# Kernel optimization log

Measured on AMD Instinct MI355X. Metric: run time of the kernel, lower is better.

The kernel has to match this reference:

```python
import jax, jax.numpy as jnp
import numpy as np

N = 500000   # query points
C = 10       # candidate faces per query (cand_num)
V = 100000   # mesh vertices
F = 200000   # mesh faces
EPS = 1e-9

def _dot(a, b):
    return jnp.sum(a * b, axis=-1)

def _proj_edge(v, e, p):
    # torch project_edge: dot(p - v, e) / clamp_min(dot(e, e), 1e-9)
    return _dot(p - v, e) / jnp.maximum(_dot(e, e), EPS)

def _is_not_above(v, e, n, p):
    # torch is_not_above: dot(cross(n, e), p - v) <= 0
    return _dot(jnp.cross(n, e), p - v) <= 0.0


def setup_inputs() -> dict:
    key = jax.random.key(0)
    k1, k2, k3, k4 = jax.random.split(key, 4)
    return {
        "query_xyz": jax.random.normal(k1, (N, 3), jnp.float32),
        "temp_verts": jax.random.normal(k2, (V, 3), jnp.float32),
        "faces": jax.random.randint(k3, (F, 3), 0, V),
        "cand_ids": jax.random.randint(k4, (N, C), 0, F),
    }


def _merged_distance(query_xyz, temp_verts, faces, cand_ids):
    # gather candidate face vertices: [N, C, 3(verts), 3(xyz)]
    fv = temp_verts[faces[cand_ids]]
    q = query_xyz[:, None, :]                       # [N, 1, 3]
    v0, v1, v2 = fv[:, :, 0, :], fv[:, :, 1, :], fv[:, :, 2, :]
    e10 = v1 - v0
    e21 = v2 - v1
    e02 = v0 - v2
    fN = -jnp.cross(e10, e02)                       # face normal (unnormalized)

    uab = _proj_edge(v0, e10, q)                    # [N, C]
    ubc = _proj_edge(v1, e21, q)
    uca = _proj_edge(v2, e02, q)

    t1 = (uca > 1.0) & (uab < 0.0)
    t2 = (uab > 1.0) & (ubc < 0.0)
    t3 = (ubc > 1.0) & (uca < 0.0)
    t4 = (uab >= 0.0) & (uab <= 1.0) & _is_not_above(v0, e10, fN, q)
    t5 = (ubc >= 0.0) & (ubc <= 1.0) & _is_not_above(v1, e21, fN, q) & ~t4
    t6 = (uca >= 0.0) & (uca <= 1.0) & _is_not_above(v2, e02, fN, q) & ~t4 & ~t5
    t0 = ~(t1 | t2 | t3 | t4 | t5 | t6)

    # type 0: signed distance to face plane (project_plane directed_dist)
    unit_n = fN / jnp.maximum(jnp.linalg.norm(fN, axis=-1, keepdims=True), EPS)
    d0 = _dot(q - v0, unit_n)

    # types 1-3: distance to vertices
    d1 = jnp.sqrt(jnp.sum((q - v0) ** 2, -1))
    d2 = jnp.sqrt(jnp.sum((q - v1) ** 2, -1))
    d3 = jnp.sqrt(jnp.sum((q - v2) ** 2, -1))

    # types 4-6: distance to edge projection points
    p4 = v0 + e10 * uab[..., None]
    p5 = v1 + e21 * ubc[..., None]
    p6 = v2 + e02 * uca[..., None]
    d4 = jnp.sqrt(jnp.sum((q - p4) ** 2, -1))
    d5 = jnp.sqrt(jnp.sum((q - p5) ** 2, -1))
    d6 = jnp.sqrt(jnp.sum((q - p6) ** 2, -1))

    f32 = lambda m: m.astype(d0.dtype)
    merged = (d0 * f32(t0) + d1 * f32(t1) + d2 * f32(t2) + d3 * f32(t3)
              + d4 * f32(t4) + d5 * f32(t5) + d6 * f32(t6))   # [N, C]

    min_idx = jnp.argmin(jnp.abs(merged), axis=-1)              # [N]
    ret = jnp.take_along_axis(cand_ids, min_idx[:, None], axis=1)[:, 0]
    md = jnp.take_along_axis(merged, min_idx[:, None], axis=1)[:, 0]
    return ret, md


def reference(query_xyz, temp_verts, faces, cand_ids):
    # Faithful translation of wootGlobalToLocal.compute_closet_faces:
    # returns (closest face id per query, signed merged distance).
    ret, md = _merged_distance(query_xyz, temp_verts, faces, cand_ids)
    return ret, md
```

## Files before the change

kernel.cpp:

```cpp
#include <hip/hip_runtime.h>
#include <math.h>

#define C_CAND 10

typedef float vf3 __attribute__((ext_vector_type(3), aligned(4)));
typedef int   vi3 __attribute__((ext_vector_type(3), aligned(4)));
typedef float v4f __attribute__((ext_vector_type(4)));

__device__ __forceinline__ float tri_merged(
    float qx, float qy, float qz,
    float v0x, float v0y, float v0z,
    float v1x, float v1y, float v1z,
    float v2x, float v2y, float v2z)
{
#pragma clang fp contract(off)
    const float e10x = v1x - v0x, e10y = v1y - v0y, e10z = v1z - v0z;
    const float e21x = v2x - v1x, e21y = v2y - v1y, e21z = v2z - v1z;
    const float e02x = v0x - v2x, e02y = v0y - v2y, e02z = v0z - v2z;

    const float crx = e10y*e02z - e10z*e02y;
    const float cry = e10z*e02x - e10x*e02z;
    const float crz = e10x*e02y - e10y*e02x;
    const float fNx = -crx, fNy = -cry, fNz = -crz;

    const float a0x = qx - v0x, a0y = qy - v0y, a0z = qz - v0z;
    const float a1x = qx - v1x, a1y = qy - v1y, a1z = qz - v1z;
    const float a2x = qx - v2x, a2y = qy - v2y, a2z = qz - v2z;

    const float num_ab = (a0x*e10x + a0y*e10y) + a0z*e10z;
    const float den_ab = fmaxf((e10x*e10x + e10y*e10y) + e10z*e10z, 1e-9f);
    const float uab = num_ab / den_ab;

    const float num_bc = (a1x*e21x + a1y*e21y) + a1z*e21z;
    const float den_bc = fmaxf((e21x*e21x + e21y*e21y) + e21z*e21z, 1e-9f);
    const float ubc = num_bc / den_bc;

    const float num_ca = (a2x*e02x + a2y*e02y) + a2z*e02z;
    const float den_ca = fmaxf((e02x*e02x + e02y*e02y) + e02z*e02z, 1e-9f);
    const float uca = num_ca / den_ca;

    const bool t1 = (uca > 1.0f) && (uab < 0.0f);
    const bool t2 = (uab > 1.0f) && (ubc < 0.0f);
    const bool t3 = (ubc > 1.0f) && (uca < 0.0f);

    const float c0x = fNy*e10z - fNz*e10y;
    const float c0y = fNz*e10x - fNx*e10z;
    const float c0z = fNx*e10y - fNy*e10x;
    const bool na0 = ((c0x*a0x + c0y*a0y) + c0z*a0z) <= 0.0f;

    const float c1x = fNy*e21z - fNz*e21y;
    const float c1y = fNz*e21x - fNx*e21z;
    const float c1z = fNx*e21y - fNy*e21x;
    const bool na1 = ((c1x*a1x + c1y*a1y) + c1z*a1z) <= 0.0f;

    const float c2x = fNy*e02z - fNz*e02y;
    const float c2y = fNz*e02x - fNx*e02z;
    const float c2z = fNx*e02y - fNy*e02x;
    const bool na2 = ((c2x*a2x + c2y*a2y) + c2z*a2z) <= 0.0f;

    const bool t4 = (uab >= 0.0f) && (uab <= 1.0f) && na0;
    const bool t5 = (ubc >= 0.0f) && (ubc <= 1.0f) && na1 && !t4;
    const bool t6 = (uca >= 0.0f) && (uca <= 1.0f) && na2 && !t4 && !t5;
    const bool t0 = !(t1 || t2 || t3 || t4 || t5 || t6);

    const float nrm = sqrtf((fNx*fNx + fNy*fNy) + fNz*fNz);
    const float dnm = fmaxf(nrm, 1e-9f);
    const float unx = fNx / dnm;
    const float uny = fNy / dnm;
    const float unz = fNz / dnm;

    const float d0 = (a0x*unx + a0y*uny) + a0z*unz;
    const float d1 = sqrtf((a0x*a0x + a0y*a0y) + a0z*a0z);
    const float d2 = sqrtf((a1x*a1x + a1y*a1y) + a1z*a1z);
    const float d3 = sqrtf((a2x*a2x + a2y*a2y) + a2z*a2z);

    const float p4x = v0x + e10x*uab, p4y = v0y + e10y*uab, p4z = v0z + e10z*uab;
    const float p5x = v1x + e21x*ubc, p5y = v1y + e21y*ubc, p5z = v1z + e21z*ubc;
    const float p6x = v2x + e02x*uca, p6y = v2y + e02y*uca, p6z = v2z + e02z*uca;

    const float g4x = qx - p4x, g4y = qy - p4y, g4z = qz - p4z;
    const float g5x = qx - p5x, g5y = qy - p5y, g5z = qz - p5z;
    const float g6x = qx - p6x, g6y = qy - p6y, g6z = qz - p6z;

    const float d4 = sqrtf((g4x*g4x + g4y*g4y) + g4z*g4z);
    const float d5 = sqrtf((g5x*g5x + g5y*g5y) + g5z*g5z);
    const float d6 = sqrtf((g6x*g6x + g6y*g6y) + g6z*g6z);

    float merged = d0 * (t0 ? 1.0f : 0.0f);
    merged = merged + d1 * (t1 ? 1.0f : 0.0f);
    merged = merged + d2 * (t2 ? 1.0f : 0.0f);
    merged = merged + d3 * (t3 ? 1.0f : 0.0f);
    merged = merged + d4 * (t4 ? 1.0f : 0.0f);
    merged = merged + d5 * (t5 ? 1.0f : 0.0f);
    merged = merged + d6 * (t6 ? 1.0f : 0.0f);
    return merged;
}

__global__ __launch_bounds__(256) void pack_faces_kernel(
    const float* __restrict__ temp_verts,
    const int*   __restrict__ faces,
    float*       __restrict__ packed,
    int F)
{
    int t = blockIdx.x * blockDim.x + threadIdx.x;
    if (t >= F) return;

    const vi3 fi = *(const vi3*)(faces + 3*t);
    const vf3 v0 = *(const vf3*)(temp_verts + 3*fi.x);
    const vf3 v1 = *(const vf3*)(temp_verts + 3*fi.y);
    const vf3 v2 = *(const vf3*)(temp_verts + 3*fi.z);

    v4f* dst = (v4f*)(packed + (size_t)16 * t);
    v4f a; a.x = v0.x; a.y = v0.y; a.z = v0.z; a.w = v1.x;
    v4f b; b.x = v1.y; b.y = v1.z; b.z = v2.x; b.w = v2.y;
    v4f c; c.x = v2.z; c.y = 0.0f; c.z = 0.0f; c.w = 0.0f;
    dst[0] = a; dst[1] = b; dst[2] = c;
}

__global__ __launch_bounds__(256) void woot_main_kernel(
    const float* __restrict__ query_xyz,
    const float* __restrict__ packed,
    const int*   __restrict__ cand_ids,
    float*       __restrict__ out_ret,
    float*       __restrict__ out_md,
    int n)
{
    int i = blockIdx.x * blockDim.x + threadIdx.x;
    if (i >= n) return;

    const vf3 q = __builtin_nontemporal_load((const vf3*)(query_xyz + 3*i));
    const float qx = q.x, qy = q.y, qz = q.z;

    float best_abs = 0.0f;
    float best_md  = 0.0f;
    int   best_f   = 0;

#pragma unroll 2
    for (int j = 0; j < C_CAND; ++j) {
        const int f = __builtin_nontemporal_load(&cand_ids[i * C_CAND + j]);

        const v4f* rp = (const v4f*)(packed + (size_t)16 * f);
        const v4f r0 = rp[0];
        const v4f r1 = rp[1];
        const v4f r2 = rp[2];

        const float merged = tri_merged(qx, qy, qz,
                                        r0.x, r0.y, r0.z,
                                        r0.w, r1.x, r1.y,
                                        r1.z, r1.w, r2.x);
        const float am = fabsf(merged);
        if (j == 0 || am < best_abs) {
            best_abs = am;
            best_md  = merged;
            best_f   = f;
        }
    }

    __builtin_nontemporal_store((float)best_f, &out_ret[i]);
    __builtin_nontemporal_store(best_md,       &out_md[i]);
}

__global__ __launch_bounds__(256) void woot_direct_kernel(
    const float* __restrict__ query_xyz,
    const float* __restrict__ temp_verts,
    const int*   __restrict__ faces,
    const int*   __restrict__ cand_ids,
    float*       __restrict__ out_ret,
    float*       __restrict__ out_md,
    int n)
{
    int i = blockIdx.x * blockDim.x + threadIdx.x;
    if (i >= n) return;

    const vf3 q = __builtin_nontemporal_load((const vf3*)(query_xyz + 3*i));
    const float qx = q.x, qy = q.y, qz = q.z;

    float best_abs = 0.0f;
    float best_md  = 0.0f;
    int   best_f   = 0;

    for (int j = 0; j < C_CAND; ++j) {
        const int f = __builtin_nontemporal_load(&cand_ids[i * C_CAND + j]);
        const vi3 fi = *(const vi3*)(faces + 3*f);
        const vf3 v0 = *(const vf3*)(temp_verts + 3*fi.x);
        const vf3 v1 = *(const vf3*)(temp_verts + 3*fi.y);
        const vf3 v2 = *(const vf3*)(temp_verts + 3*fi.z);

        const float merged = tri_merged(qx, qy, qz,
                                        v0.x, v0.y, v0.z,
                                        v1.x, v1.y, v1.z,
                                        v2.x, v2.y, v2.z);
        const float am = fabsf(merged);
        if (j == 0 || am < best_abs) {
            best_abs = am;
            best_md  = merged;
            best_f   = f;
        }
    }

    __builtin_nontemporal_store((float)best_f, &out_ret[i]);
    __builtin_nontemporal_store(best_md,       &out_md[i]);
}

extern "C" void kernel_launch(void* const* d_in, const int* in_sizes, int n_in,
                              void* d_out, int out_size, void* d_ws, size_t ws_size,
                              hipStream_t stream) {
    const float* query_xyz  = (const float*)d_in[0];
    const float* temp_verts = (const float*)d_in[1];
    const int*   faces      = (const int*)d_in[2];
    const int*   cand_ids   = (const int*)d_in[3];

    const int n = in_sizes[0] / 3;
    const int F = in_sizes[2] / 3;

    float* out_ret = (float*)d_out;
    float* out_md  = out_ret + n;

    const int block = 256;
    const int grid_n = (n + block - 1) / block;

    const size_t need = (size_t)F * 16 * sizeof(float);
    if (ws_size >= need) {
        float* packed = (float*)d_ws;
        const int grid_f = (F + block - 1) / block;
        pack_faces_kernel<<<grid_f, block, 0, stream>>>(
            temp_verts, faces, packed, F);
        woot_main_kernel<<<grid_n, block, 0, stream>>>(
            query_xyz, packed, cand_ids, out_ret, out_md, n);
    } else {
        woot_direct_kernel<<<grid_n, block, 0, stream>>>(
            query_xyz, temp_verts, faces, cand_ids, out_ret, out_md, n);
    }
}
```

Baseline: 174.9 us.

## Slice face range across blocks and reduce argmin with 64-bit atomicMin

Adds a sliced path that splits faces into four index ranges. Each block handles one slice for 256 queries: it compacts the candidates that fall in its slice into a per-wave shared queue and evaluates them, then combines per-query results through atomicMin on a packed (|dist|, j, f) key. A final resolve kernel recomputes the signed distance for the winning face. The goal is better cache locality on the packed-face gathers, since each slice touches only a quarter of the face table. The cost is two extra kernel launches, reading cand_ids four times, global atomics and a recompute pass. Ties now resolve by smallest (j, f) key instead of first-seen order.

```diff
diff --git a/kernel.cpp b/kernel.cpp
--- a/kernel.cpp
+++ b/kernel.cpp
@@ -117,6 +117,112 @@
     dst[0] = a; dst[1] = b; dst[2] = c;
 }
 
+__global__ __launch_bounds__(256) void fill_keys_kernel(
+    unsigned long long* __restrict__ keys, int n)
+{
+    int i = blockIdx.x * blockDim.x + threadIdx.x;
+    if (i < n) keys[i] = ~0ull;
+}
+
+__global__ __launch_bounds__(256) void woot_sliced_kernel(
+    const float* __restrict__ query_xyz,
+    const float* __restrict__ packed,
+    const int*   __restrict__ cand_ids,
+    unsigned long long* __restrict__ keys,
+    int n, int Fs, int F)
+{
+    const int slice  = blockIdx.x & 3;
+    const int qblock = blockIdx.x >> 2;
+    const int tid    = threadIdx.x;
+    const int lane   = tid & 63;
+    const int wid    = tid >> 6;
+    const int qi     = qblock * 256 + tid;
+
+    __shared__ float qs0[256], qs1[256], qs2[256];
+    __shared__ unsigned int queue[4][640];
+
+    const int lo = slice * Fs;
+    const int hi = (lo + Fs < F) ? (lo + Fs) : F;
+
+    const bool valid = qi < n;
+    if (valid) {
+        const vf3 q = __builtin_nontemporal_load((const vf3*)(query_xyz + 3*qi));
+        qs0[tid] = q.x; qs1[tid] = q.y; qs2[tid] = q.z;
+    }
+
+    unsigned int cnt = 0;
+    for (int j = 0; j < C_CAND; ++j) {
+        int f = -1;
+        if (valid) f = __builtin_nontemporal_load(&cand_ids[qi * C_CAND + j]);
+        const bool in = valid && (f >= lo) && (f < hi);
+        const unsigned long long m = __ballot(in);
+        if (in) {
+            const unsigned long long below = (1ull << lane) - 1ull;
+            const unsigned int pos = cnt + (unsigned)__popcll(m & below);
+            queue[wid][pos] = (unsigned)f | ((unsigned)j << 18)
+                                          | ((unsigned)lane << 22);
+        }
+        cnt += (unsigned)__popcll(m);
+    }
+
+    __syncthreads();
+
+    for (unsigned int base = 0; base < cnt; base += 64) {
+        const unsigned int idx = base + (unsigned)lane;
+        const bool act = idx < cnt;
+        const unsigned int e = act ? queue[wid][idx] : 0u;
+        const int f    = (int)(e & 0x3FFFFu);
+        const int j    = (int)((e >> 18) & 0xFu);
+        const int qloc = wid * 64 + (int)((e >> 22) & 0x3Fu);
+        const float QX = qs0[qloc], QY = qs1[qloc], QZ = qs2[qloc];
+
+        if (act) {
+            const v4f* rp = (const v4f*)(packed + (size_t)16 * f);
+            const v4f r0 = rp[0];
+            const v4f r1 = rp[1];
+            const v4f r2 = rp[2];
+            const float merged = tri_merged(QX, QY, QZ,
+                                            r0.x, r0.y, r0.z,
+                                            r0.w, r1.x, r1.y,
+                                            r1.z, r1.w, r2.x);
+            const float am = fabsf(merged);
+            const unsigned long long key =
+                ((unsigned long long)__float_as_uint(am) << 32)
+                | ((unsigned long long)(unsigned)j << 18)
+                | (unsigned long long)(unsigned)f;
+            atomicMin(&keys[qblock * 256 + qloc], key);
+        }
+    }
+}
+
+__global__ __launch_bounds__(256) void resolve_kernel(
+    const float* __restrict__ query_xyz,
+    const float* __restrict__ packed,
+    const unsigned long long* __restrict__ keys,
+    float* __restrict__ out_ret,
+    float* __restrict__ out_md,
+    int n)
+{
+    int i = blockIdx.x * blockDim.x + threadIdx.x;
+    if (i >= n) return;
+
+    const unsigned long long k = keys[i];
+    const int f = (int)(k & 0x3FFFFu);
+
+    const vf3 q = __builtin_nontemporal_load((const vf3*)(query_xyz + 3*i));
+    const v4f* rp = (const v4f*)(packed + (size_t)16 * f);
+    const v4f r0 = rp[0];
+    const v4f r1 = rp[1];
+    const v4f r2 = rp[2];
+    const float merged = tri_merged(q.x, q.y, q.z,
+                                    r0.x, r0.y, r0.z,
+                                    r0.w, r1.x, r1.y,
+                                    r1.z, r1.w, r2.x);
+
+    __builtin_nontemporal_store((float)f, &out_ret[i]);
+    __builtin_nontemporal_store(merged,   &out_md[i]);
+}
+
 __global__ __launch_bounds__(256) void woot_main_kernel(
     const float* __restrict__ query_xyz,
     const float* __restrict__ packed,
@@ -129,31 +235,22 @@
     if (i >= n) return;
 
     const vf3 q = __builtin_nontemporal_load((const vf3*)(query_xyz + 3*i));
-    const float qx = q.x, qy = q.y, qz = q.z;
-
-    float best_abs = 0.0f;
-    float best_md  = 0.0f;
-    int   best_f   = 0;
+    float best_abs = 0.0f, best_md = 0.0f;
+    int best_f = 0;
 
 #pragma unroll 2
     for (int j = 0; j < C_CAND; ++j) {
         const int f = __builtin_nontemporal_load(&cand_ids[i * C_CAND + j]);
-
         const v4f* rp = (const v4f*)(packed + (size_t)16 * f);
         const v4f r0 = rp[0];
         const v4f r1 = rp[1];
         const v4f r2 = rp[2];
-
-        const float merged = tri_merged(qx, qy, qz,
+        const float merged = tri_merged(q.x, q.y, q.z,
                                         r0.x, r0.y, r0.z,
                                         r0.w, r1.x, r1.y,
                                         r1.z, r1.w, r2.x);
         const float am = fabsf(merged);
-        if (j == 0 || am < best_abs) {
-            best_abs = am;
-            best_md  = merged;
-            best_f   = f;
-        }
+        if (j == 0 || am < best_abs) { best_abs = am; best_md = merged; best_f = f; }
     }
 
     __builtin_nontemporal_store((float)best_f, &out_ret[i]);
@@ -173,11 +270,8 @@
     if (i >= n) return;
 
     const vf3 q = __builtin_nontemporal_load((const vf3*)(query_xyz + 3*i));
-    const float qx = q.x, qy = q.y, qz = q.z;
-
-    float best_abs = 0.0f;
-    float best_md  = 0.0f;
-    int   best_f   = 0;
+    float best_abs = 0.0f, best_md = 0.0f;
+    int best_f = 0;
 
     for (int j = 0; j < C_CAND; ++j) {
         const int f = __builtin_nontemporal_load(&cand_ids[i * C_CAND + j]);
@@ -185,17 +279,12 @@
         const vf3 v0 = *(const vf3*)(temp_verts + 3*fi.x);
         const vf3 v1 = *(const vf3*)(temp_verts + 3*fi.y);
         const vf3 v2 = *(const vf3*)(temp_verts + 3*fi.z);
-
-        const float merged = tri_merged(qx, qy, qz,
+        const float merged = tri_merged(q.x, q.y, q.z,
                                         v0.x, v0.y, v0.z,
                                         v1.x, v1.y, v1.z,
                                         v2.x, v2.y, v2.z);
         const float am = fabsf(merged);
-        if (j == 0 || am < best_abs) {
-            best_abs = am;
-            best_md  = merged;
-            best_f   = f;
-        }
+        if (j == 0 || am < best_abs) { best_abs = am; best_md = merged; best_f = f; }
     }
 
     __builtin_nontemporal_store((float)best_f, &out_ret[i]);
@@ -216,13 +305,28 @@
     float* out_ret = (float*)d_out;
     float* out_md  = out_ret + n;
 
-    const int block = 256;
+    const int block  = 256;
     const int grid_n = (n + block - 1) / block;
-
-    const size_t need = (size_t)F * 16 * sizeof(float);
-    if (ws_size >= need) {
+    const int grid_f = (F + block - 1) / block;
+
+    const size_t need_pack   = (size_t)F * 16 * sizeof(float);
+    const size_t need_sliced = need_pack + (size_t)n * sizeof(unsigned long long);
+
+    if (ws_size >= need_sliced && F < (1 << 18)) {
         float* packed = (float*)d_ws;
-        const int grid_f = (F + block - 1) / block;
+        unsigned long long* keys =
+            (unsigned long long*)((char*)d_ws + need_pack);
+        const int Fs = (F + 3) / 4;
+
+        pack_faces_kernel<<<grid_f, block, 0, stream>>>(
+            temp_verts, faces, packed, F);
+        fill_keys_kernel<<<grid_n, block, 0, stream>>>(keys, n);
+        woot_sliced_kernel<<<grid_n * 4, block, 0, stream>>>(
+            query_xyz, packed, cand_ids, keys, n, Fs, F);
+        resolve_kernel<<<grid_n, block, 0, stream>>>(
+            query_xyz, packed, keys, out_ret, out_md, n);
+    } else if (ws_size >= need_pack) {
+        float* packed = (float*)d_ws;
         pack_faces_kernel<<<grid_f, block, 0, stream>>>(
             temp_verts, faces, packed, F);
         woot_main_kernel<<<grid_n, block, 0, stream>>>(
```

Result: slower. 236.0 us (+34.9%).
